# Performance work log

Measured on AMD Instinct MI355X. Metric: run time of the kernel, lower is better.

The kernel has to match this reference:

```python
import jax, jax.numpy as jnp
import numpy as np

EMB = 1024
HEADS = 16
HEAD_DIM = EMB // HEADS
N = 16384


def setup_inputs() -> dict:
    key = jax.random.key(0)
    ks = jax.random.split(key, 9)
    s = 1.0 / np.sqrt(EMB)
    return {
        "src": jax.random.normal(ks[0], (N, EMB), dtype=jnp.float32),
        "Wq": jax.random.normal(ks[1], (EMB, EMB), dtype=jnp.float32) * s,
        "bq": jax.random.normal(ks[2], (EMB,), dtype=jnp.float32) * s,
        "Wk": jax.random.normal(ks[3], (EMB, EMB), dtype=jnp.float32) * s,
        "bk": jax.random.normal(ks[4], (EMB,), dtype=jnp.float32) * s,
        "Wv": jax.random.normal(ks[5], (EMB, EMB), dtype=jnp.float32) * s,
        "bv": jax.random.normal(ks[6], (EMB,), dtype=jnp.float32) * s,
        "Wo": jax.random.normal(ks[7], (EMB, EMB), dtype=jnp.float32) * s,
        "bo": jax.random.normal(ks[8], (EMB,), dtype=jnp.float32) * s,
    }


def reference(src, Wq, bq, Wk, bk, Wv, bv, Wo, bo):
    # nn.Linear: y = x @ W^T + b  (W is [out, in])
    q = src @ Wq.T + bq          # [N, E]
    k = src @ Wk.T + bk
    v = src @ Wv.T + bv
    q = q.reshape(-1, HEADS, HEAD_DIM)   # [N, H, D]
    k = k.reshape(-1, HEADS, HEAD_DIM)
    v = v.reshape(-1, HEADS, HEAD_DIM)
    # NOTE: attention is across heads within each token: scores [N, H, H]
    scale = 1.0 / jnp.sqrt(jnp.float32(HEAD_DIM))
    scores = jnp.einsum('nhd,ngd->nhg', q, k) * scale   # [N, H, H]
    attn = jax.nn.softmax(scores, axis=-1)
    out = jnp.einsum('nhg,ngd->nhd', attn, v)            # [N, H, D]
    out = out.reshape(-1, EMB)
    out = out @ Wo.T + bo                                 # [N, E]
    return out.reshape(-1, HEADS, HEAD_DIM)               # [N, H, D]
```

## Files before the change

kernel.cpp:

```cpp
#include <hip/hip_runtime.h>
#include <stdint.h>
#include <stddef.h>

#define EMB 1024
#define NTOK 16384

typedef __attribute__((ext_vector_type(8))) short short8;
typedef __attribute__((ext_vector_type(4))) float floatx4;

__device__ __forceinline__ unsigned short f2bf(float f) {
    union { float f; unsigned int u; } v; v.f = f;
    unsigned int u = v.u;
    unsigned int r = (u + 0x7fffu + ((u >> 16) & 1u)) >> 16;
    return (unsigned short)r;
}
__device__ __forceinline__ float bf2f(unsigned short s) {
    union { unsigned int u; float f; } v; v.u = ((unsigned int)s) << 16;
    return v.f;
}

__device__ __forceinline__ void gload16(const void* g, void* l) {
    __builtin_amdgcn_global_load_lds(
        (const __attribute__((address_space(1))) void*)g,
        (__attribute__((address_space(3))) void*)l, 16, 0, 0);
}

#define DSR(dst, base, imm) \
    asm volatile("ds_read_b128 %0, %1 offset:%c2" : "=v"(dst) : "v"(base), "i"(imm))

__global__ void cvt_kernel(const float* __restrict__ in,
                           unsigned short* __restrict__ out, int n4) {
    int idx = blockIdx.x * blockDim.x + threadIdx.x;
    int stride = gridDim.x * blockDim.x;
    for (int i = idx; i < n4; i += stride) {
        float4 f = reinterpret_cast<const float4*>(in)[i];
        ushort4 o;
        o.x = f2bf(f.x); o.y = f2bf(f.y); o.z = f2bf(f.z); o.w = f2bf(f.w);
        reinterpret_cast<ushort4*>(out)[i] = o;
    }
}

__global__ void cvt4_kernel(const float* __restrict__ s0, const float* __restrict__ s1,
                            const float* __restrict__ s2, const float* __restrict__ s3,
                            unsigned short* __restrict__ out) {
    int idx = blockIdx.x * blockDim.x + threadIdx.x;
    const int total = 4 << 18;
    int stride = gridDim.x * blockDim.x;
    for (int i = idx; i < total; i += stride) {
        int w = i >> 18, r = i & ((1 << 18) - 1);
        const float* s = (w == 0) ? s0 : (w == 1) ? s1 : (w == 2) ? s2 : s3;
        float4 f = reinterpret_cast<const float4*>(s)[r];
        ushort4 o;
        o.x = f2bf(f.x); o.y = f2bf(f.y); o.z = f2bf(f.z); o.w = f2bf(f.w);
        reinterpret_cast<ushort4*>(out)[i] = o;
    }
}

__global__ void bias_cat_kernel(const float* __restrict__ b0,
                                const float* __restrict__ b1,
                                const float* __restrict__ b2,
                                float* __restrict__ out) {
    int i = blockIdx.x * blockDim.x + threadIdx.x;
    float v = (i < 1024) ? b0[i] : (i < 2048 ? b1[i - 1024] : b2[i - 2048]);
    out[i] = v;
}

__device__ __forceinline__ void store_val(float* C, size_t idx, float v) { C[idx] = v; }
__device__ __forceinline__ void store_val(unsigned short* C, size_t idx, float v) { C[idx] = f2bf(v); }

template<typename OUT_T>
__global__ __launch_bounds__(512, 2)
void gemm256(const unsigned short* __restrict__ A,
             const unsigned short* __restrict__ B,
             const float* __restrict__ bias,
             OUT_T* __restrict__ C,
             int K, int Nc, int grid_m)
{
    __shared__ unsigned short lds[65536];

    const int bid = blockIdx.x;
    const int x = bid & 7;
    const int w = bid >> 3;
    const int ms = grid_m >> 3;
    const int m0 = (x * ms + (w & (ms - 1))) * 256;
    const int n0 = (w / ms) * 256;

    const int tid  = threadIdx.x;
    const int lane = tid & 63;
    const int wid  = tid >> 6;
    const int wm = (wid >> 2) * 128;
    const int wn = (wid & 3) * 64;
    const int rr = lane & 15;
    const int klo = (((lane >> 4) ^ ((rr >> 1) & 3)) << 3);

    const int aro = (wm + rr) * 32 + klo;
    const int bro = 16384 + (wn + rr) * 32 + klo;

    const unsigned ldsb = (unsigned)(uintptr_t)(void*)&lds[0];

    const unsigned short* pA[2];
    const unsigned short* pB[2];
    int ldst[2];
#pragma unroll
    for (int l = 0; l < 2; ++l) {
        const int P16  = l * 512 + tid;
        const int rowS = P16 >> 2;
        const int colel = (((P16 & 3) ^ ((rowS >> 1) & 3)) << 3);
        pA[l] = A + (size_t)(m0 + rowS) * K + colel;
        pB[l] = B + (size_t)(n0 + rowS) * K + colel;
        ldst[l] = P16 * 8;
    }

    floatx4 acc[8][4];
#pragma unroll
    for (int i = 0; i < 8; ++i)
#pragma unroll
        for (int j = 0; j < 4; ++j)
            acc[i][j] = (floatx4){0.f, 0.f, 0.f, 0.f};

    const int NT = K >> 6;

#pragma unroll
    for (int l = 0; l < 2; ++l) {
        gload16(pA[l],      &lds[0     + ldst[l]]);
        gload16(pA[l] + 32, &lds[8192  + ldst[l]]);
        gload16(pB[l],      &lds[16384 + ldst[l]]);
        gload16(pB[l] + 32, &lds[24576 + ldst[l]]);
    }
    __builtin_amdgcn_sched_barrier(0);
    asm volatile("s_waitcnt vmcnt(0)");
    __builtin_amdgcn_s_barrier();
    __builtin_amdgcn_sched_barrier(0);

    for (int t = 0; t < NT; ++t) {
        const int cur = (t & 1) * 32768;
        const int nxt = cur ^ 32768;
        const int ktn = (t + 1 < NT) ? (t + 1) * 64 : 0;
        const unsigned abA = ldsb + (unsigned)(2 * (cur + aro));
        const unsigned abB = ldsb + (unsigned)(2 * (cur + bro));

        short8 a0[4], a1[4], bb[4];

        gload16(pA[0] + ktn, &lds[nxt + ldst[0]]);
        gload16(pA[1] + ktn, &lds[nxt + ldst[1]]);
        gload16(pB[0] + ktn, &lds[nxt + 16384 + ldst[0]]);
        gload16(pB[1] + ktn, &lds[nxt + 16384 + ldst[1]]);
        DSR(a0[0], abA, 0);    DSR(a0[1], abA, 1024);
        DSR(a0[2], abA, 2048); DSR(a0[3], abA, 3072);
        DSR(bb[0], abB, 0);    DSR(bb[1], abB, 1024);
        DSR(bb[2], abB, 2048); DSR(bb[3], abB, 3072);
        DSR(a1[0], abA, 4096); DSR(a1[1], abA, 5120);
        DSR(a1[2], abA, 6144); DSR(a1[3], abA, 7168);
        asm volatile("s_waitcnt lgkmcnt(0)");
        __builtin_amdgcn_sched_barrier(0);
        __builtin_amdgcn_s_setprio(1);
#pragma unroll
        for (int j = 0; j < 4; ++j)
#pragma unroll
            for (int i = 0; i < 4; ++i)
                acc[i][j] = __builtin_amdgcn_mfma_f32_16x16x32_bf16(a0[i], bb[j], acc[i][j], 0, 0, 0);
#pragma unroll
        for (int j = 0; j < 4; ++j)
#pragma unroll
            for (int i = 0; i < 4; ++i)
                acc[4 + i][j] = __builtin_amdgcn_mfma_f32_16x16x32_bf16(a1[i], bb[j], acc[4 + i][j], 0, 0, 0);
        __builtin_amdgcn_s_setprio(0);
        __builtin_amdgcn_sched_barrier(0);
        asm volatile("s_waitcnt vmcnt(4)");
        __builtin_amdgcn_s_barrier();
        __builtin_amdgcn_sched_barrier(0);

        gload16(pA[0] + ktn + 32, &lds[nxt + 8192 + ldst[0]]);
        gload16(pA[1] + ktn + 32, &lds[nxt + 8192 + ldst[1]]);
        gload16(pB[0] + ktn + 32, &lds[nxt + 24576 + ldst[0]]);
        gload16(pB[1] + ktn + 32, &lds[nxt + 24576 + ldst[1]]);
        DSR(a0[0], abA, 16384 + 0);    DSR(a0[1], abA, 16384 + 1024);
        DSR(a0[2], abA, 16384 + 2048); DSR(a0[3], abA, 16384 + 3072);
        DSR(bb[0], abB, 16384 + 0);    DSR(bb[1], abB, 16384 + 1024);
        DSR(bb[2], abB, 16384 + 2048); DSR(bb[3], abB, 16384 + 3072);
        DSR(a1[0], abA, 20480 + 0);    DSR(a1[1], abA, 20480 + 1024);
        DSR(a1[2], abA, 20480 + 2048); DSR(a1[3], abA, 20480 + 3072);
        asm volatile("s_waitcnt lgkmcnt(0)");
        __builtin_amdgcn_sched_barrier(0);
        __builtin_amdgcn_s_setprio(1);
#pragma unroll
        for (int j = 0; j < 4; ++j)
#pragma unroll
            for (int i = 0; i < 4; ++i)
                acc[i][j] = __builtin_amdgcn_mfma_f32_16x16x32_bf16(a0[i], bb[j], acc[i][j], 0, 0, 0);
#pragma unroll
        for (int j = 0; j < 4; ++j)
#pragma unroll
            for (int i = 0; i < 4; ++i)
                acc[4 + i][j] = __builtin_amdgcn_mfma_f32_16x16x32_bf16(a1[i], bb[j], acc[4 + i][j], 0, 0, 0);
        __builtin_amdgcn_s_setprio(0);
        __builtin_amdgcn_sched_barrier(0);
        asm volatile("s_waitcnt vmcnt(4)");
        __builtin_amdgcn_s_barrier();
        __builtin_amdgcn_sched_barrier(0);
    }

    const int cn  = lane & 15;
    const int cm4 = (lane >> 4) * 4;
    float bv[4];
#pragma unroll
    for (int j = 0; j < 4; ++j) bv[j] = bias[n0 + wn + j * 16 + cn];
#pragma unroll
    for (int ai = 0; ai < 8; ++ai) {
        const int row = m0 + wm + (ai >> 2) * 64 + (ai & 3) * 16 + cm4;
#pragma unroll
        for (int j = 0; j < 4; ++j) {
            const int col = n0 + wn + j * 16 + cn;
#pragma unroll
            for (int r = 0; r < 4; ++r)
                store_val(C, (size_t)(row + r) * Nc + col, acc[ai][j][r] + bv[j]);
        }
    }
}

#define ROWP 72

__global__ __launch_bounds__(256)
void attn_kernel(const unsigned short* __restrict__ QKV,
                 unsigned short* __restrict__ O)
{
    const int wave = threadIdx.x >> 6;
    const int lane = threadIdx.x & 63;
    const int n = blockIdx.x * 4 + wave;

    __shared__ unsigned short lq[4][16 * ROWP];
    __shared__ unsigned short lk[4][16 * ROWP];
    __shared__ unsigned short lv[4][16 * ROWP];
    __shared__ float lp[4][256];

    {
        const unsigned short* gq = QKV + (size_t)n * 3072;
        const unsigned short* gk = gq + 1024;
        const unsigned short* gv = gq + 2048;
        for (int t = lane; t < 128; t += 64) {
            int r = t >> 3, c = t & 7;
            *reinterpret_cast<short8*>(&lq[wave][r * ROWP + c * 8]) =
                *reinterpret_cast<const short8*>(gq + t * 8);
            *reinterpret_cast<short8*>(&lk[wave][r * ROWP + c * 8]) =
                *reinterpret_cast<const short8*>(gk + t * 8);
            *reinterpret_cast<short8*>(&lv[wave][r * ROWP + c * 8]) =
                *reinterpret_cast<const short8*>(gv + t * 8);
        }
    }
    __syncthreads();

    const int g = lane & 15;
    const int a = lane >> 4;

    float kf[64];
#pragma unroll
    for (int c2 = 0; c2 < 8; ++c2) {
        short8 kv = *reinterpret_cast<const short8*>(&lk[wave][g * ROWP + c2 * 8]);
#pragma unroll
        for (int e = 0; e < 8; ++e) kf[c2 * 8 + e] = bf2f((unsigned short)kv[e]);
    }

#pragma unroll
    for (int i = 0; i < 4; ++i) {
        const int h = i * 4 + a;
        float s = 0.f;
#pragma unroll
        for (int c2 = 0; c2 < 8; ++c2) {
            short8 qv = *reinterpret_cast<const short8*>(&lq[wave][h * ROWP + c2 * 8]);
#pragma unroll
            for (int e = 0; e < 8; ++e)
                s = fmaf(bf2f((unsigned short)qv[e]), kf[c2 * 8 + e], s);
        }
        s *= 0.125f;

        float m = s;
#pragma unroll
        for (int o = 1; o < 16; o <<= 1) m = fmaxf(m, __shfl_xor(m, o, 64));
        float p = expf(s - m);
        float sum = p;
#pragma unroll
        for (int o = 1; o < 16; o <<= 1) sum += __shfl_xor(sum, o, 64);
        lp[wave][h * 16 + g] = p / sum;
    }
    __syncthreads();

    const int h = lane >> 2;
    const int db = (lane & 3) * 16;
    float o[16];
#pragma unroll
    for (int e = 0; e < 16; ++e) o[e] = 0.f;

    for (int g2 = 0; g2 < 16; ++g2) {
        const float pw = lp[wave][h * 16 + g2];
        short8 v0 = *reinterpret_cast<const short8*>(&lv[wave][g2 * ROWP + db]);
        short8 v1 = *reinterpret_cast<const short8*>(&lv[wave][g2 * ROWP + db + 8]);
#pragma unroll
        for (int e = 0; e < 8; ++e) {
            o[e]     = fmaf(pw, bf2f((unsigned short)v0[e]), o[e]);
            o[8 + e] = fmaf(pw, bf2f((unsigned short)v1[e]), o[8 + e]);
        }
    }

    short8 o0, o1;
#pragma unroll
    for (int e = 0; e < 8; ++e) {
        o0[e] = (short)f2bf(o[e]);
        o1[e] = (short)f2bf(o[8 + e]);
    }
    unsigned short* dst = O + (size_t)n * EMB + h * 64 + db;
    *reinterpret_cast<short8*>(dst) = o0;
    *reinterpret_cast<short8*>(dst + 8) = o1;
}

extern "C" void kernel_launch(void* const* d_in, const int* in_sizes, int n_in,
                              void* d_out, int out_size, void* d_ws, size_t ws_size,
                              hipStream_t stream)
{
    const float* src = (const float*)d_in[0];
    const float* Wq  = (const float*)d_in[1];
    const float* bq  = (const float*)d_in[2];
    const float* Wk  = (const float*)d_in[3];
    const float* bk  = (const float*)d_in[4];
    const float* Wv  = (const float*)d_in[5];
    const float* bv  = (const float*)d_in[6];
    const float* Wo  = (const float*)d_in[7];
    const float* bo  = (const float*)d_in[8];
    float* out = (float*)d_out;

    unsigned short* ws = (unsigned short*)d_ws;
    unsigned short* src_bf = ws;
    unsigned short* wqkv   = src_bf + (size_t)NTOK * EMB;
    unsigned short* wo_bf  = wqkv + (size_t)3 * EMB * EMB;
    unsigned short* qkv    = wo_bf + (size_t)EMB * EMB;
    unsigned short* ab     = qkv + (size_t)NTOK * 3 * EMB;
    float* bias_cat        = (float*)(ab + (size_t)NTOK * EMB);

    cvt_kernel<<<2048, 256, 0, stream>>>(src, src_bf, NTOK * EMB / 4);
    cvt4_kernel<<<2048, 256, 0, stream>>>(Wq, Wk, Wv, Wo, wqkv);
    bias_cat_kernel<<<12, 256, 0, stream>>>(bq, bk, bv, bias_cat);

    gemm256<unsigned short><<<dim3(64 * 12), 512, 0, stream>>>(
        src_bf, wqkv, bias_cat, qkv, EMB, 3 * EMB, 64);

    attn_kernel<<<NTOK / 4, 256, 0, stream>>>(qkv, ab);

    gemm256<float><<<dim3(64 * 4), 512, 0, stream>>>(
        ab, wo_bf, bo, out, EMB, EMB, 64);
}
```

Before: 200.7 us.

## Rewrite GEMM main loop as 8-phase ping-pong schedule with 128B swizzled LDS

Replaces the two-half K-loop of the 256x256 bf16 GEMM with a four-quadrant, barrier-synchronised schedule. Each phase interleaves LDS fragment reads, one global-to-LDS staging chunk and a quarter of the MFMA work, and B tiles are prefetched two iterations ahead. The LDS layout moves to 64-wide K rows with an 8-way XOR swizzle, and launch bounds drop to one block per CU. The aim is to hide LDS and global latency behind MFMA issue. The cost is many more s_barriers, a different occupancy, and a tricky staging order that must stay correct.

Measured after the change: 197.7 us. No clear change (-1.5%).

```diff
diff --git a/kernel.cpp b/kernel.cpp
--- a/kernel.cpp
+++ b/kernel.cpp
@@ -25,8 +25,10 @@
         (__attribute__((address_space(3))) void*)l, 16, 0, 0);
 }
 
+#define SB0() __builtin_amdgcn_sched_barrier(0)
+
 #define DSR(dst, base, imm) \
-    asm volatile("ds_read_b128 %0, %1 offset:%c2" : "=v"(dst) : "v"(base), "i"(imm))
+    asm volatile("ds_read_b128 %0, %1 offset:%c2" : "=&v"(dst) : "v"(base), "i"(imm))
 
 __global__ void cvt_kernel(const float* __restrict__ in,
                            unsigned short* __restrict__ out, int n4) {
@@ -68,13 +70,29 @@
 __device__ __forceinline__ void store_val(float* C, size_t idx, float v) { C[idx] = v; }
 __device__ __forceinline__ void store_val(unsigned short* C, size_t idx, float v) { C[idx] = f2bf(v); }
 
+#define STG_A(h, bf, ko) do { \
+    gload16(pA + (h)*KH + (ko),       &lds[(bf)*32768 + (h)*8192 + ldT]);  \
+    gload16(pA + (h)*KH + (ko) + K64, &lds[(bf)*32768 + (h)*8192 + ldT2]); } while (0)
+#define STG_B(h, bf, ko) do { \
+    gload16(pB + (h)*KH + (ko),       &lds[(bf)*32768 + 16384 + (h)*8192 + ldT]);  \
+    gload16(pB + (h)*KH + (ko) + K64, &lds[(bf)*32768 + 16384 + (h)*8192 + ldT2]); } while (0)
+
+#define QMFMA(MB, NB, BF) do { \
+    _Pragma("unroll") \
+    for (int j_ = 0; j_ < 2; ++j_) { \
+        _Pragma("unroll") \
+        for (int i_ = 0; i_ < 4; ++i_) { \
+            acc[(MB)+i_][(NB)+j_] = __builtin_amdgcn_mfma_f32_16x16x32_bf16(ak0[i_], BF[j_*2],   acc[(MB)+i_][(NB)+j_], 0, 0, 0); \
+            acc[(MB)+i_][(NB)+j_] = __builtin_amdgcn_mfma_f32_16x16x32_bf16(ak1[i_], BF[j_*2+1], acc[(MB)+i_][(NB)+j_], 0, 0, 0); \
+        } } } while (0)
+
 template<typename OUT_T>
-__global__ __launch_bounds__(512, 2)
-void gemm256(const unsigned short* __restrict__ A,
-             const unsigned short* __restrict__ B,
-             const float* __restrict__ bias,
-             OUT_T* __restrict__ C,
-             int K, int Nc, int grid_m)
+__global__ __launch_bounds__(512, 1)
+void gemm8p(const unsigned short* __restrict__ A,
+            const unsigned short* __restrict__ B,
+            const float* __restrict__ bias,
+            OUT_T* __restrict__ C,
+            int K, int Nc, int grid_m)
 {
     __shared__ unsigned short lds[65536];
 
@@ -85,31 +103,24 @@
     const int m0 = (x * ms + (w & (ms - 1))) * 256;
     const int n0 = (w / ms) * 256;
 
-    const int tid  = threadIdx.x;
-    const int lane = tid & 63;
-    const int wid  = tid >> 6;
-    const int wm = (wid >> 2) * 128;
-    const int wn = (wid & 3) * 64;
-    const int rr = lane & 15;
-    const int klo = (((lane >> 4) ^ ((rr >> 1) & 3)) << 3);
-
-    const int aro = (wm + rr) * 32 + klo;
-    const int bro = 16384 + (wn + rr) * 32 + klo;
+    const int tid = threadIdx.x, lane = tid & 63, wid = tid >> 6;
+    const int wm = (wid >> 2) * 128, wn = (wid & 3) * 64;
+    const int rr = lane & 15, ls = lane >> 4;
+    const int sw0 = ((ls)     ^ (rr & 7)) << 4;
+    const int sw1 = ((4 | ls) ^ (rr & 7)) << 4;
 
     const unsigned ldsb = (unsigned)(uintptr_t)(void*)&lds[0];
-
-    const unsigned short* pA[2];
-    const unsigned short* pB[2];
-    int ldst[2];
-#pragma unroll
-    for (int l = 0; l < 2; ++l) {
-        const int P16  = l * 512 + tid;
-        const int rowS = P16 >> 2;
-        const int colel = (((P16 & 3) ^ ((rowS >> 1) & 3)) << 3);
-        pA[l] = A + (size_t)(m0 + rowS) * K + colel;
-        pB[l] = B + (size_t)(n0 + rowS) * K + colel;
-        ldst[l] = P16 * 8;
-    }
+    const unsigned aB0 = ldsb + (unsigned)((wm >> 7) * 16384 + rr * 128 + sw0);
+    const unsigned aB1 = ldsb + (unsigned)((wm >> 7) * 16384 + rr * 128 + sw1);
+    const unsigned bB0 = ldsb + 32768u + (unsigned)((wn >> 7) * 16384 + (wn & 64) * 128 + rr * 128 + sw0);
+    const unsigned bB1 = ldsb + 32768u + (unsigned)((wn >> 7) * 16384 + (wn & 64) * 128 + rr * 128 + sw1);
+
+    const int rT = tid >> 3, gst = tid & 7;
+    const int gsrc = (gst ^ (rT & 7)) * 8;
+    const unsigned short* pA = A + (size_t)(m0 + rT) * K + gsrc;
+    const unsigned short* pB = B + (size_t)(n0 + rT) * K + gsrc;
+    const int K64 = K * 64, KH = K * 128;
+    const int ldT = tid * 8, ldT2 = (tid + 512) * 8;
 
     floatx4 acc[8][4];
 #pragma unroll
@@ -120,84 +131,82 @@
 
     const int NT = K >> 6;
 
-#pragma unroll
-    for (int l = 0; l < 2; ++l) {
-        gload16(pA[l],      &lds[0     + ldst[l]]);
-        gload16(pA[l] + 32, &lds[8192  + ldst[l]]);
-        gload16(pB[l],      &lds[16384 + ldst[l]]);
-        gload16(pB[l] + 32, &lds[24576 + ldst[l]]);
-    }
-    __builtin_amdgcn_sched_barrier(0);
-    asm volatile("s_waitcnt vmcnt(0)");
+    STG_A(0, 0, 0); STG_A(1, 0, 0); STG_B(0, 0, 0); STG_B(1, 0, 0);
+    STG_B(0, 1, 64); STG_B(1, 1, 64);
+    SB0();
+    asm volatile("s_waitcnt vmcnt(4)");
     __builtin_amdgcn_s_barrier();
-    __builtin_amdgcn_sched_barrier(0);
+    SB0();
+
+    short8 ak0[4], ak1[4], b0f[4], b1f[4];
 
     for (int t = 0; t < NT; ++t) {
-        const int cur = (t & 1) * 32768;
-        const int nxt = cur ^ 32768;
-        const int ktn = (t + 1 < NT) ? (t + 1) * 64 : 0;
-        const unsigned abA = ldsb + (unsigned)(2 * (cur + aro));
-        const unsigned abB = ldsb + (unsigned)(2 * (cur + bro));
-
-        short8 a0[4], a1[4], bb[4];
-
-        gload16(pA[0] + ktn, &lds[nxt + ldst[0]]);
-        gload16(pA[1] + ktn, &lds[nxt + ldst[1]]);
-        gload16(pB[0] + ktn, &lds[nxt + 16384 + ldst[0]]);
-        gload16(pB[1] + ktn, &lds[nxt + 16384 + ldst[1]]);
-        DSR(a0[0], abA, 0);    DSR(a0[1], abA, 1024);
-        DSR(a0[2], abA, 2048); DSR(a0[3], abA, 3072);
-        DSR(bb[0], abB, 0);    DSR(bb[1], abB, 1024);
-        DSR(bb[2], abB, 2048); DSR(bb[3], abB, 3072);
-        DSR(a1[0], abA, 4096); DSR(a1[1], abA, 5120);
-        DSR(a1[2], abA, 6144); DSR(a1[3], abA, 7168);
+        const int bfc = t & 1, bfn = bfc ^ 1;
+        const unsigned cB = (unsigned)(bfc * 65536);
+        const unsigned aC0 = aB0 + cB, aC1 = aB1 + cB;
+        const unsigned bC0 = bB0 + cB, bC1 = bB1 + cB;
+        const int ko1 = ((t + 1 < NT) ? (t + 1) : 0) * 64;
+        const int ko2 = ((t + 2 < NT) ? (t + 2) : (t + 2 - NT)) * 64;
+
+        DSR(ak0[0], aC0, 0);    DSR(ak0[1], aC0, 2048);
+        DSR(ak0[2], aC0, 4096); DSR(ak0[3], aC0, 6144);
+        DSR(ak1[0], aC1, 0);    DSR(ak1[1], aC1, 2048);
+        DSR(ak1[2], aC1, 4096); DSR(ak1[3], aC1, 6144);
+        DSR(b0f[0], bC0, 0);    DSR(b0f[1], bC1, 0);
+        DSR(b0f[2], bC0, 2048); DSR(b0f[3], bC1, 2048);
+        STG_A(0, bfn, ko1);
+        SB0();
+        __builtin_amdgcn_s_barrier();
         asm volatile("s_waitcnt lgkmcnt(0)");
-        __builtin_amdgcn_sched_barrier(0);
+        SB0();
         __builtin_amdgcn_s_setprio(1);
-#pragma unroll
-        for (int j = 0; j < 4; ++j)
-#pragma unroll
-            for (int i = 0; i < 4; ++i)
-                acc[i][j] = __builtin_amdgcn_mfma_f32_16x16x32_bf16(a0[i], bb[j], acc[i][j], 0, 0, 0);
-#pragma unroll
-        for (int j = 0; j < 4; ++j)
-#pragma unroll
-            for (int i = 0; i < 4; ++i)
-                acc[4 + i][j] = __builtin_amdgcn_mfma_f32_16x16x32_bf16(a1[i], bb[j], acc[4 + i][j], 0, 0, 0);
+        QMFMA(0, 0, b0f);
         __builtin_amdgcn_s_setprio(0);
-        __builtin_amdgcn_sched_barrier(0);
+        SB0();
+        __builtin_amdgcn_s_barrier();
+        SB0();
+
+        DSR(b1f[0], bC0, 4096); DSR(b1f[1], bC1, 4096);
+        DSR(b1f[2], bC0, 6144); DSR(b1f[3], bC1, 6144);
+        STG_A(1, bfn, ko1);
+        SB0();
+        __builtin_amdgcn_s_barrier();
+        asm volatile("s_waitcnt lgkmcnt(0)");
+        SB0();
+        __builtin_amdgcn_s_setprio(1);
+        QMFMA(0, 2, b1f);
+        __builtin_amdgcn_s_setprio(0);
+        SB0();
+        __builtin_amdgcn_s_barrier();
+        SB0();
+
+        DSR(ak0[0], aC0, 8192);  DSR(ak0[1], aC0, 10240);
+        DSR(ak0[2], aC0, 12288); DSR(ak0[3], aC0, 14336);
+        DSR(ak1[0], aC1, 8192);  DSR(ak1[1], aC1, 10240);
+        DSR(ak1[2], aC1, 12288); DSR(ak1[3], aC1, 14336);
+        STG_B(0, bfc, ko2);
+        SB0();
+        __builtin_amdgcn_s_barrier();
+        asm volatile("s_waitcnt lgkmcnt(0)");
+        SB0();
+        __builtin_amdgcn_s_setprio(1);
+        QMFMA(4, 2, b1f);
+        __builtin_amdgcn_s_setprio(0);
+        SB0();
+        __builtin_amdgcn_s_barrier();
+        SB0();
+
+        STG_B(1, bfc, ko2);
+        SB0();
+        __builtin_amdgcn_s_barrier();
+        SB0();
+        __builtin_amdgcn_s_setprio(1);
+        QMFMA(4, 0, b0f);
+        __builtin_amdgcn_s_setprio(0);
+        SB0();
         asm volatile("s_waitcnt vmcnt(4)");
         __builtin_amdgcn_s_barrier();
-        __builtin_amdgcn_sched_barrier(0);
-
-        gload16(pA[0] + ktn + 32, &lds[nxt + 8192 + ldst[0]]);
-        gload16(pA[1] + ktn + 32, &lds[nxt + 8192 + ldst[1]]);
-        gload16(pB[0] + ktn + 32, &lds[nxt + 24576 + ldst[0]]);
-        gload16(pB[1] + ktn + 32, &lds[nxt + 24576 + ldst[1]]);
-        DSR(a0[0], abA, 16384 + 0);    DSR(a0[1], abA, 16384 + 1024);
-        DSR(a0[2], abA, 16384 + 2048); DSR(a0[3], abA, 16384 + 3072);
-        DSR(bb[0], abB, 16384 + 0);    DSR(bb[1], abB, 16384 + 1024);
-        DSR(bb[2], abB, 16384 + 2048); DSR(bb[3], abB, 16384 + 3072);
-        DSR(a1[0], abA, 20480 + 0);    DSR(a1[1], abA, 20480 + 1024);
-        DSR(a1[2], abA, 20480 + 2048); DSR(a1[3], abA, 20480 + 3072);
-        asm volatile("s_waitcnt lgkmcnt(0)");
-        __builtin_amdgcn_sched_barrier(0);
-        __builtin_amdgcn_s_setprio(1);
-#pragma unroll
-        for (int j = 0; j < 4; ++j)
-#pragma unroll
-            for (int i = 0; i < 4; ++i)
-                acc[i][j] = __builtin_amdgcn_mfma_f32_16x16x32_bf16(a0[i], bb[j], acc[i][j], 0, 0, 0);
-#pragma unroll
-        for (int j = 0; j < 4; ++j)
-#pragma unroll
-            for (int i = 0; i < 4; ++i)
-                acc[4 + i][j] = __builtin_amdgcn_mfma_f32_16x16x32_bf16(a1[i], bb[j], acc[4 + i][j], 0, 0, 0);
-        __builtin_amdgcn_s_setprio(0);
-        __builtin_amdgcn_sched_barrier(0);
-        asm volatile("s_waitcnt vmcnt(4)");
-        __builtin_amdgcn_s_barrier();
-        __builtin_amdgcn_sched_barrier(0);
+        SB0();
     }
 
     const int cn  = lane & 15;
@@ -339,11 +348,11 @@
     cvt4_kernel<<<2048, 256, 0, stream>>>(Wq, Wk, Wv, Wo, wqkv);
     bias_cat_kernel<<<12, 256, 0, stream>>>(bq, bk, bv, bias_cat);
 
-    gemm256<unsigned short><<<dim3(64 * 12), 512, 0, stream>>>(
+    gemm8p<unsigned short><<<dim3(64 * 12), 512, 0, stream>>>(
         src_bf, wqkv, bias_cat, qkv, EMB, 3 * EMB, 64);
 
     attn_kernel<<<NTOK / 4, 256, 0, stream>>>(qkv, ab);
 
-    gemm256<float><<<dim3(64 * 4), 512, 0, stream>>>(
+    gemm8p<float><<<dim3(64 * 4), 512, 0, stream>>>(
         ab, wo_bf, bo, out, EMB, EMB, 64);
 }
```
